# Kernel tuning notes

Hardware: AMD Instinct MI355X
Metric: run time of the kernel (lower is better)

The kernel has to match this reference:

```python
import jax, jax.numpy as jnp
import numpy as np

BETA = 0.25
DECAY = 0.99
EPS = 1e-05
K = 1024        # num_codebook_vectors
D = 256         # latent_dim


def setup_inputs() -> dict:
    key = jax.random.key(0)
    k1, k2, k3 = jax.random.split(key, 3)
    return {
        "z": jax.random.normal(k1, (32, D, 32, 32), dtype=jnp.float32),
        "embedding": jax.random.normal(k2, (K, D), dtype=jnp.float32),
        "ema_cluster_size": jnp.zeros((K,), dtype=jnp.float32),
        "ema_w": jax.random.normal(k3, (K, D), dtype=jnp.float32),
    }


def reference(z, embedding, ema_cluster_size, ema_w):
    B, C, H, W = z.shape
    zp = jnp.transpose(z, (0, 2, 3, 1))            # [B,H,W,C]
    zf = zp.reshape(-1, C)                          # [N, D], N = B*H*W

    # squared L2 distances: ||z||^2 + ||e||^2 - 2 z e^T  -> [N, K]
    d = (jnp.sum(zf * zf, axis=1, keepdims=True)
         + jnp.sum(embedding * embedding, axis=1)
         - 2.0 * (zf @ embedding.T))
    idx = jnp.argmin(d, axis=1)                     # [N]

    # one-hot @ embedding == gather of codebook rows
    z_q = embedding[idx].reshape(zp.shape)          # [B,H,W,C]

    # EMA codebook update (training branch)
    counts = jnp.zeros((K,), dtype=zf.dtype).at[idx].add(1.0)   # encodings.sum(0)
    cs = ema_cluster_size * DECAY + (1.0 - DECAY) * counts
    n = jnp.sum(cs)
    cs = (cs + EPS) / (n + K * EPS) * n             # Laplace smoothing
    dw = jax.ops.segment_sum(zf, idx, num_segments=K)           # encodings.T @ zf
    new_ema_w = ema_w * DECAY + (1.0 - DECAY) * dw
    new_embedding = new_ema_w / cs[:, None]

    # commitment loss + straight-through estimator
    e_latent_loss = jnp.mean((jax.lax.stop_gradient(z_q) - zp) ** 2)
    loss = BETA * e_latent_loss
    z_q_st = zp + jax.lax.stop_gradient(z_q - zp)
    z_q_out = jnp.transpose(z_q_st, (0, 3, 1, 2))   # [B,C,H,W]

    return z_q_out, idx[:, None], loss, new_embedding, cs, new_ema_w
```

## Files before the change

### kernel.cpp

```cpp
#include <hip/hip_runtime.h>

typedef unsigned long long ull;
typedef __attribute__((ext_vector_type(8))) short bf16x8;
typedef __attribute__((ext_vector_type(4))) float f32x4;
typedef __attribute__((ext_vector_type(8))) unsigned short u16x8;

#define DECAY 0.99f
#define BETA 0.25f
#define EPSV 1e-5f
#define EPSGAP 0.0625f

#define Dd 256
#define Kk 1024
#define Nn 32768
#define ZELEM 8388608

__device__ __forceinline__ unsigned short f2bf(float f) {
    unsigned int x = __float_as_uint(f);
    x += 0x7FFFu + ((x >> 16) & 1u);
    return (unsigned short)(x >> 16);
}
__device__ __forceinline__ float bf2f(unsigned short b) {
    return __uint_as_float(((unsigned int)b) << 16);
}
__device__ __forceinline__ unsigned mono(unsigned b) {
    return b ^ (((int)b >> 31) | 0x80000000u);
}
__device__ __forceinline__ float unmono(unsigned m) {
    unsigned b = (m & 0x80000000u) ? (m ^ 0x80000000u) : ~m;
    return __uint_as_float(b);
}
__device__ __forceinline__ unsigned umin32(unsigned a, unsigned b) { return a < b ? a : b; }
__device__ __forceinline__ unsigned umax32(unsigned a, unsigned b) { return a > b ? a : b; }

__global__ __launch_bounds__(256) void prep_e_kernel(
        const float* __restrict__ emb, unsigned short* __restrict__ ehg,
        unsigned short* __restrict__ elg, float* __restrict__ esq,
        int* __restrict__ hist, int* __restrict__ flagcnt,
        float* __restrict__ loss_fix) {
    const int nsub = blockIdx.x;
    const int t = threadIdx.x;
    if (t < 16) hist[nsub * 16 + t] = 0;
    if (nsub == 0 && t == 16) flagcnt[0] = 0;
    if (nsub == 0 && t == 17) loss_fix[0] = 0.0f;
    #pragma unroll
    for (int it = 0; it < 2; ++it) {
        const int item = it * 256 + t;
        const int kc = item >> 6, lane = item & 63;
        const int quad = lane >> 4, nl = lane & 15;
        const float* ep = emb + (size_t)(nsub * 16 + nl) * Dd + kc * 32 + quad * 8;
        const float4 a = *(const float4*)ep;
        const float4 b4 = *(const float4*)(ep + 4);
        const float v[8] = {a.x, a.y, a.z, a.w, b4.x, b4.y, b4.z, b4.w};
        u16x8 hi, lo;
        #pragma unroll
        for (int j = 0; j < 8; ++j) {
            const unsigned short h = f2bf(v[j]);
            hi[j] = h;
            lo[j] = f2bf(v[j] - bf2f(h));
        }
        const size_t off = ((size_t)(nsub * 8 + kc) * 64 + lane) * 8;
        *(u16x8*)&ehg[off] = hi;
        *(u16x8*)&elg[off] = lo;
    }
    {
        const int nl = t >> 4, seg = t & 15;
        const float* ep = emb + (size_t)(nsub * 16 + nl) * Dd + seg * 16;
        float s = 0.0f;
        #pragma unroll
        for (int j = 0; j < 4; ++j) {
            const float4 v4 = *(const float4*)(ep + j * 4);
            s += v4.x * v4.x + v4.y * v4.y + v4.z * v4.z + v4.w * v4.w;
        }
        #pragma unroll
        for (int d = 1; d < 16; d <<= 1) s += __shfl_xor(s, d);
        if (seg == 0) esq[nsub * 16 + nl] = s;
    }
}

__global__ __launch_bounds__(256) void dist_kernel(
        const float* __restrict__ z, const unsigned short* __restrict__ ehg,
        const unsigned short* __restrict__ elg, const float* __restrict__ esq,
        const float* __restrict__ emb,
        float* __restrict__ zq, float* __restrict__ dwr, int repmask,
        int* __restrict__ idx_i, float* __restrict__ idx_f,
        int* __restrict__ hist, int* __restrict__ flagcnt,
        int* __restrict__ flaglist, float* __restrict__ flagval,
        float* __restrict__ loss_p) {
    __shared__ __align__(16) unsigned char smem[70656];
    __shared__ int kidx[64];
    unsigned short* zh = (unsigned short*)smem;
    unsigned short* zl = (unsigned short*)(smem + 32768);
    ull* mb   = (ull*)(smem + 65536);
    ull* ms   = (ull*)(smem + 67584);
    float* zsqp = (float*)(smem + 69632);
    float* eldsf = (float*)smem;

    const int t = threadIdx.x, w = t >> 6, L = t & 63;
    const int quad = L >> 4, lr = L & 15;
    const int m0 = blockIdx.x * 64;
    const int b = m0 >> 10, hw0 = m0 & 1023;

    {
        const int c0 = w * 64;
        const float* zp = z + (size_t)b * 262144 + hw0 + L;
        float s = 0.0f;
        #pragma unroll
        for (int cg = 0; cg < 8; ++cg) {
            float v[8];
            #pragma unroll
            for (int j = 0; j < 8; ++j)
                v[j] = zp[(size_t)(c0 + cg * 8 + j) * 1024];
            u16x8 hi, lo;
            #pragma unroll
            for (int j = 0; j < 8; ++j) {
                s = fmaf(v[j], v[j], s);
                const unsigned short h = f2bf(v[j]);
                hi[j] = h;
                lo[j] = f2bf(v[j] - bf2f(h));
            }
            const int chunk = ((c0 >> 3) + cg) ^ (L & 7);
            *(u16x8*)&zh[L * 256 + chunk * 8] = hi;
            *(u16x8*)&zl[L * 256 + chunk * 8] = lo;
        }
        zsqp[L * 4 + w] = s;
    }
    __syncthreads();

    const unsigned short* ehw = ehg + (size_t)(w * 1024 + L) * 8;
    const unsigned short* elw = elg + (size_t)(w * 1024 + L) * 8;

    unsigned bb[16], ss[16];
    #pragma unroll
    for (int i = 0; i < 16; ++i) { bb[i] = 0xFFFFFFFFu; ss[i] = 0xFFFFFFFFu; }

    bf16x8 Bh[2][2], Bl[2][2];
    #pragma unroll
    for (int ni = 0; ni < 2; ++ni) {
        Bh[0][ni] = *(const bf16x8*)(ehw + (size_t)ni * 4096);
        Bl[0][ni] = *(const bf16x8*)(elw + (size_t)ni * 4096);
    }
    bf16x8 Ah[2][4], Al[2][4];
    #pragma unroll
    for (int mi = 0; mi < 4; ++mi) {
        const int chunk = quad ^ (lr & 7);
        const int o = (mi * 16 + lr) * 256 + chunk * 8;
        Ah[0][mi] = *(const bf16x8*)&zh[o];
        Al[0][mi] = *(const bf16x8*)&zl[o];
    }

    for (int nt = 0; nt < 8; ++nt) {
        f32x4 acc[4][2];
        #pragma unroll
        for (int mi = 0; mi < 4; ++mi)
            #pragma unroll
            for (int ni = 0; ni < 2; ++ni) acc[mi][ni] = (f32x4){0.f, 0.f, 0.f, 0.f};

        #pragma unroll
        for (int kc = 0; kc < 8; ++kc) {
            const int cur = kc & 1, nxt = cur ^ 1;
            const int nkc = (kc + 1) & 7;
            const int nnt = (kc == 7) ? ((nt + 1) & 7) : nt;
            #pragma unroll
            for (int ni = 0; ni < 2; ++ni) {
                const size_t o = (size_t)nnt * 32768 + (size_t)ni * 4096 + (size_t)nkc * 512;
                Bh[nxt][ni] = *(const bf16x8*)(ehw + o);
                Bl[nxt][ni] = *(const bf16x8*)(elw + o);
            }
            #pragma unroll
            for (int mi = 0; mi < 4; ++mi) {
                const int chunk = (nkc * 4 + quad) ^ (lr & 7);
                const int o = (mi * 16 + lr) * 256 + chunk * 8;
                Ah[nxt][mi] = *(const bf16x8*)&zh[o];
                Al[nxt][mi] = *(const bf16x8*)&zl[o];
            }
            __builtin_amdgcn_s_setprio(1);
            #pragma unroll
            for (int mi = 0; mi < 4; ++mi)
                #pragma unroll
                for (int ni = 0; ni < 2; ++ni) {
                    acc[mi][ni] = __builtin_amdgcn_mfma_f32_16x16x32_bf16(Ah[cur][mi], Bh[cur][ni], acc[mi][ni], 0, 0, 0);
                    acc[mi][ni] = __builtin_amdgcn_mfma_f32_16x16x32_bf16(Ah[cur][mi], Bl[cur][ni], acc[mi][ni], 0, 0, 0);
                    acc[mi][ni] = __builtin_amdgcn_mfma_f32_16x16x32_bf16(Al[cur][mi], Bh[cur][ni], acc[mi][ni], 0, 0, 0);
                }
            __builtin_amdgcn_s_setprio(0);
        }
        const int q0 = nt * 8 + w * 2;
        const float e0b = esq[q0 * 16 + lr] + 512.0f;
        const float e1b = esq[(q0 + 1) * 16 + lr] + 512.0f;
        #pragma unroll
        for (int mi = 0; mi < 4; ++mi)
            #pragma unroll
            for (int reg = 0; reg < 4; ++reg) {
                const int i = mi * 4 + reg;
                #pragma unroll
                for (int ni = 0; ni < 2; ++ni) {
                    const float val = fmaf(-2.0f, acc[mi][ni][reg], ni ? e1b : e0b);
                    const unsigned pk = (__float_as_uint(val) & 0xFFFFFFC0u) | (unsigned)(q0 + ni);
                    const unsigned mx = umax32(bb[i], pk);
                    bb[i] = umin32(bb[i], pk);
                    ss[i] = umin32(ss[i], mx);
                }
            }
    }

    #pragma unroll
    for (int mi = 0; mi < 4; ++mi)
        #pragma unroll
        for (int reg = 0; reg < 4; ++reg) {
            const int i = mi * 4 + reg;
            ull b2 = ((ull)(bb[i] & 0xFFFFFFC0u) << 14) | (ull)((bb[i] & 63u) * 16 + lr);
            ull s2 = ((ull)(ss[i] & 0xFFFFFFC0u) << 14) | (ull)((ss[i] & 63u) * 16 + lr);
            #pragma unroll
            for (int d = 1; d < 16; d <<= 1) {
                const ull ob = __shfl_xor(b2, d);
                const ull os = __shfl_xor(s2, d);
                const ull mx = ob < b2 ? b2 : ob;
                b2 = ob < b2 ? ob : b2;
                const ull ns = os < s2 ? os : s2;
                s2 = mx < ns ? mx : ns;
            }
            if (lr == 0) {
                const int row = mi * 16 + quad * 4 + reg;
                mb[w * 64 + row] = b2;
                ms[w * 64 + row] = s2;
            }
        }
    __syncthreads();

    if (t < 64) {
        ull b2 = mb[t], s2 = ms[t];
        #pragma unroll
        for (int ww = 1; ww < 4; ++ww) {
            const ull ob = mb[ww * 64 + t], os = ms[ww * 64 + t];
            const ull mx = ob < b2 ? b2 : ob;
            b2 = ob < b2 ? ob : b2;
            const ull ns = os < s2 ? os : s2;
            s2 = mx < ns ? mx : ns;
        }
        const int k = (int)(b2 & 16383ull);
        const float v1 = __uint_as_float((unsigned)(b2 >> 14)) - 512.0f;
        const float v2 = __uint_as_float((unsigned)(s2 >> 14)) - 512.0f;
        idx_i[m0 + t] = k;
        idx_f[m0 + t] = (float)k;
        kidx[t] = k;
        atomicAdd(&hist[k], 1);
        if (v2 - v1 < EPSGAP) {
            const int pos = atomicAdd(flagcnt, 1);
            flaglist[pos] = m0 + t;
            flagval[pos] = v1;
        }
        float lp = v1 + zsqp[t * 4] + zsqp[t * 4 + 1] + zsqp[t * 4 + 2] + zsqp[t * 4 + 3];
        #pragma unroll
        for (int d = 32; d > 0; d >>= 1) lp += __shfl_down(lp, d);
        if (t == 0) loss_p[blockIdx.x] = lp;
    }
    __syncthreads();

    for (int pr = w; pr < 64; pr += 4) {
        const float* er = emb + (size_t)kidx[pr] * Dd;
        #pragma unroll
        for (int g = 0; g < 4; ++g)
            eldsf[pr * 257 + g * 64 + L] = er[g * 64 + L];
    }
    __syncthreads();

    {
        const int g = t & 15;
        const int cl = t >> 4;
        float* zqb = zq + (size_t)b * 262144 + hw0 + g * 4;
        #pragma unroll
        for (int pass = 0; pass < 16; ++pass) {
            const int c = pass * 16 + cl;
            float4 v;
            v.x = eldsf[(g * 4 + 0) * 257 + c];
            v.y = eldsf[(g * 4 + 1) * 257 + c];
            v.z = eldsf[(g * 4 + 2) * 257 + c];
            v.w = eldsf[(g * 4 + 3) * 257 + c];
            *(float4*)(zqb + (size_t)c * 1024) = v;
        }
    }

    {
        const int c = t;
        const float* zcol = z + (size_t)b * 262144 + (size_t)c * 1024 + hw0;
        float* dwb = dwr + (size_t)(blockIdx.x & repmask) * (Kk * Dd);
        #pragma unroll 4
        for (int p = 0; p < 64; ++p) {
            atomicAdd(&dwb[(size_t)kidx[p] * Dd + c], zcol[p]);
        }
    }
}

__global__ __launch_bounds__(256) void fixup_kernel(
        const float* __restrict__ z, const float* __restrict__ emb,
        const float* __restrict__ esq, const int* __restrict__ flagcnt,
        const int* __restrict__ flaglist, const float* __restrict__ flagval,
        int* __restrict__ idx_i, float* __restrict__ idx_f,
        int* __restrict__ hist, float* __restrict__ loss_fix,
        float* __restrict__ zq, float* __restrict__ dw) {
    __shared__ float zrow[256];
    __shared__ ull red[256];
    __shared__ int s_pair[2];
    const int t = threadIdx.x;
    const int total = flagcnt[0];
    for (int fi = blockIdx.x; fi < total; fi += 512) {
        const int n = flaglist[fi];
        const int b = n >> 10, hw = n & 1023;
        __syncthreads();
        zrow[t] = z[(size_t)b * 262144 + (size_t)t * 1024 + hw];
        __syncthreads();
        ull best = ~0ull;
        #pragma unroll
        for (int kc = 0; kc < 4; ++kc) {
            const int k = t * 4 + kc;
            const float* ep = emb + (size_t)k * Dd;
            float dot = 0.0f;
            #pragma unroll 8
            for (int c4 = 0; c4 < 64; ++c4) {
                const float4 e4 = *(const float4*)(ep + c4 * 4);
                const float4 z4 = *(const float4*)&zrow[c4 * 4];
                dot = fmaf(z4.x, e4.x, dot);
                dot = fmaf(z4.y, e4.y, dot);
                dot = fmaf(z4.z, e4.z, dot);
                dot = fmaf(z4.w, e4.w, dot);
            }
            const float val = esq[k] - 2.0f * dot;
            const ull pk = ((ull)mono(__float_as_uint(val)) << 32) | (unsigned)k;
            if (pk < best) best = pk;
        }
        red[t] = best;
        __syncthreads();
        for (int s = 128; s > 0; s >>= 1) {
            if (t < s) { if (red[t + s] < red[t]) red[t] = red[t + s]; }
            __syncthreads();
        }
        if (t == 0) {
            const int knew = (int)(unsigned)(red[0] & 0xFFFFFFFFull);
            const float vnew = unmono((unsigned)(red[0] >> 32));
            const int kold = idx_i[n];
            s_pair[0] = kold;
            s_pair[1] = knew;
            if (knew != kold) {
                idx_i[n] = knew;
                idx_f[n] = (float)knew;
                atomicSub(&hist[kold], 1);
                atomicAdd(&hist[knew], 1);
            }
            atomicAdd(loss_fix, vnew - flagval[fi]);
        }
        __syncthreads();
        const int kold = s_pair[0], knew = s_pair[1];
        if (knew != kold) {
            const float zv = zrow[t];
            atomicAdd(&dw[(size_t)kold * Dd + t], -zv);
            atomicAdd(&dw[(size_t)knew * Dd + t], zv);
            zq[(size_t)b * 262144 + (size_t)t * 1024 + hw] = emb[(size_t)knew * Dd + t];
        }
    }
}

__global__ void scan_fin1_kernel(const int* __restrict__ hist,
                                 const float* __restrict__ ema_cs,
                                 const float* __restrict__ loss_p,
                                 const float* __restrict__ loss_fix,
                                 float* __restrict__ cs_out,
                                 float* __restrict__ loss_out) {
    __shared__ float wred[16], wred2[16];
    const int t = threadIdx.x;
    const int w = t >> 6, lane = t & 63;
    const int v = hist[t];
    const float csr = ema_cs[t] * DECAY + (1.0f - DECAY) * (float)v;
    float r = csr;
    float r2 = (t < 512) ? loss_p[t] : 0.0f;
    #pragma unroll
    for (int d = 32; d > 0; d >>= 1) { r += __shfl_xor(r, d); r2 += __shfl_xor(r2, d); }
    if (lane == 0) { wred[w] = r; wred2[w] = r2; }
    __syncthreads();
    if (t < 16) {
        float rr = wred[t], rr2 = wred2[t];
        #pragma unroll
        for (int d = 1; d < 16; d <<= 1) { rr += __shfl_xor(rr, d); rr2 += __shfl_xor(rr2, d); }
        if (t == 0) { wred[0] = rr; wred2[0] = rr2; }
    }
    __syncthreads();
    const float nsum = wred[0];
    const float cs = (csr + EPSV) / (nsum + (float)Kk * EPSV) * nsum;
    cs_out[t] = cs;
    if (t == 0) loss_out[0] = BETA * (wred2[0] + loss_fix[0]) / (float)ZELEM;
}

__global__ __launch_bounds__(256) void finalize2_kernel(
        const float* __restrict__ ema_w, const float* __restrict__ dwr,
        int nrep, const float* __restrict__ cs_out,
        float* __restrict__ new_emb_out, float* __restrict__ new_ema_w_out) {
    const int i = blockIdx.x * 256 + threadIdx.x;
    float s = 0.0f;
    for (int r = 0; r < nrep; ++r) s += dwr[(size_t)r * (Kk * Dd) + i];
    const float nw = ema_w[i] * DECAY + (1.0f - DECAY) * s;
    const float cs = cs_out[i >> 8];
    new_ema_w_out[i] = nw;
    new_emb_out[i]   = nw / cs;
}

extern "C" void kernel_launch(void* const* d_in, const int* in_sizes, int n_in,
                              void* d_out, int out_size, void* d_ws, size_t ws_size,
                              hipStream_t stream) {
    const float* z      = (const float*)d_in[0];
    const float* emb    = (const float*)d_in[1];
    const float* ema_cs = (const float*)d_in[2];
    const float* ema_w  = (const float*)d_in[3];

    float* out = (float*)d_out;
    float* zq_out        = out;
    float* idx_out_f     = out + 8388608;
    float* loss_out      = out + 8421376;
    float* new_emb_out   = out + 8421377;
    float* cs_out        = out + 8683521;
    float* new_ema_w_out = out + 8684545;

    int*   idx_i    = (int*)d_ws;
    int*   flagcnt  = idx_i + 32768;
    float* loss_fix = (float*)(flagcnt + 16);
    int*   flaglist = (int*)(loss_fix + 16);
    float* flagval  = (float*)(flaglist + 32768);
    int*   hist     = (int*)(flagval + 32768);
    float* esq      = (float*)(hist + 1024);
    float* loss_p   = esq + 1024;
    unsigned short* ehg = (unsigned short*)(loss_p + 512);
    unsigned short* elg = ehg + 262144;
    size_t dwr_off = ((size_t)((char*)(elg + 262144) - (char*)d_ws) + 255) & ~(size_t)255;
    float* dwr = (float*)((char*)d_ws + dwr_off);
    const size_t repbytes = (size_t)Kk * Dd * 4;
    size_t rem = (ws_size > dwr_off) ? ws_size - dwr_off : 0;
    int nrep = 1;
    while (nrep < 8 && (size_t)(nrep * 2) * repbytes <= rem) nrep <<= 1;

    hipMemsetAsync(dwr, 0, (size_t)nrep * repbytes, stream);
    prep_e_kernel<<<64, 256, 0, stream>>>(emb, ehg, elg, esq, hist, flagcnt,
                                          loss_fix);
    dist_kernel<<<Nn / 64, 256, 0, stream>>>(z, ehg, elg, esq, emb, zq_out,
                                             dwr, nrep - 1, idx_i, idx_out_f,
                                             hist, flagcnt, flaglist, flagval,
                                             loss_p);
    fixup_kernel<<<512, 256, 0, stream>>>(z, emb, esq, flagcnt, flaglist,
                                          flagval, idx_i, idx_out_f, hist,
                                          loss_fix, zq_out, dwr);
    scan_fin1_kernel<<<1, 1024, 0, stream>>>(hist, ema_cs, loss_p, loss_fix,
                                             cs_out, loss_out);
    finalize2_kernel<<<Kk * Dd / 256, 256, 0, stream>>>(ema_w, dwr, nrep,
                                                        cs_out, new_emb_out,
                                                        new_ema_w_out);
}
```

Baseline: 237.0 us.

## Fold dw memset and cluster-size/loss reductions into prep and finalize kernels

Removes the separate memset of the dw replica buffers by zeroing them inside an enlarged prep kernel (512 blocks). The total cluster count is computed up front using the identity that the counts sum to N, so cs no longer needs a global reduction after the histogram. That lets the single-block scan kernel be dropped: each finalize block computes its own cs, and block 0 reduces the loss. This cuts two launches and a serialized single-block kernel, at the cost of a slightly different summation order for n.

```diff
diff --git a/kernel.cpp b/kernel.cpp
--- a/kernel.cpp
+++ b/kernel.cpp
@@ -37,44 +37,64 @@
         const float* __restrict__ emb, unsigned short* __restrict__ ehg,
         unsigned short* __restrict__ elg, float* __restrict__ esq,
         int* __restrict__ hist, int* __restrict__ flagcnt,
-        float* __restrict__ loss_fix) {
+        float* __restrict__ loss_fix, float* __restrict__ nsum,
+        const float* __restrict__ ema_cs, float* __restrict__ dwr, int nrep) {
     const int nsub = blockIdx.x;
     const int t = threadIdx.x;
-    if (t < 16) hist[nsub * 16 + t] = 0;
-    if (nsub == 0 && t == 16) flagcnt[0] = 0;
-    if (nsub == 0 && t == 17) loss_fix[0] = 0.0f;
-    #pragma unroll
-    for (int it = 0; it < 2; ++it) {
-        const int item = it * 256 + t;
-        const int kc = item >> 6, lane = item & 63;
-        const int quad = lane >> 4, nl = lane & 15;
-        const float* ep = emb + (size_t)(nsub * 16 + nl) * Dd + kc * 32 + quad * 8;
-        const float4 a = *(const float4*)ep;
-        const float4 b4 = *(const float4*)(ep + 4);
-        const float v[8] = {a.x, a.y, a.z, a.w, b4.x, b4.y, b4.z, b4.w};
-        u16x8 hi, lo;
-        #pragma unroll
-        for (int j = 0; j < 8; ++j) {
-            const unsigned short h = f2bf(v[j]);
-            hi[j] = h;
-            lo[j] = f2bf(v[j] - bf2f(h));
-        }
-        const size_t off = ((size_t)(nsub * 8 + kc) * 64 + lane) * 8;
-        *(u16x8*)&ehg[off] = hi;
-        *(u16x8*)&elg[off] = lo;
-    }
     {
-        const int nl = t >> 4, seg = t & 15;
-        const float* ep = emb + (size_t)(nsub * 16 + nl) * Dd + seg * 16;
-        float s = 0.0f;
-        #pragma unroll
-        for (int j = 0; j < 4; ++j) {
-            const float4 v4 = *(const float4*)(ep + j * 4);
-            s += v4.x * v4.x + v4.y * v4.y + v4.z * v4.z + v4.w * v4.w;
-        }
-        #pragma unroll
-        for (int d = 1; d < 16; d <<= 1) s += __shfl_xor(s, d);
-        if (seg == 0) esq[nsub * 16 + nl] = s;
+        const int per = nrep * 512;
+        float4* dst = (float4*)(dwr + (size_t)nsub * per);
+        const int n4 = per >> 2;
+        for (int j = t; j < n4; j += 256) dst[j] = make_float4(0.f, 0.f, 0.f, 0.f);
+    }
+    if (nsub < 64) {
+        if (t < 16) hist[nsub * 16 + t] = 0;
+        if (nsub == 0 && t == 16) flagcnt[0] = 0;
+        if (nsub == 0 && t == 17) loss_fix[0] = 0.0f;
+        #pragma unroll
+        for (int it = 0; it < 2; ++it) {
+            const int item = it * 256 + t;
+            const int kc = item >> 6, lane = item & 63;
+            const int quad = lane >> 4, nl = lane & 15;
+            const float* ep = emb + (size_t)(nsub * 16 + nl) * Dd + kc * 32 + quad * 8;
+            const float4 a = *(const float4*)ep;
+            const float4 b4 = *(const float4*)(ep + 4);
+            const float v[8] = {a.x, a.y, a.z, a.w, b4.x, b4.y, b4.z, b4.w};
+            u16x8 hi, lo;
+            #pragma unroll
+            for (int j = 0; j < 8; ++j) {
+                const unsigned short h = f2bf(v[j]);
+                hi[j] = h;
+                lo[j] = f2bf(v[j] - bf2f(h));
+            }
+            const size_t off = ((size_t)(nsub * 8 + kc) * 64 + lane) * 8;
+            *(u16x8*)&ehg[off] = hi;
+            *(u16x8*)&elg[off] = lo;
+        }
+        {
+            const int nl = t >> 4, seg = t & 15;
+            const float* ep = emb + (size_t)(nsub * 16 + nl) * Dd + seg * 16;
+            float s = 0.0f;
+            #pragma unroll
+            for (int j = 0; j < 4; ++j) {
+                const float4 v4 = *(const float4*)(ep + j * 4);
+                s += v4.x * v4.x + v4.y * v4.y + v4.z * v4.z + v4.w * v4.w;
+            }
+            #pragma unroll
+            for (int d = 1; d < 16; d <<= 1) s += __shfl_xor(s, d);
+            if (seg == 0) esq[nsub * 16 + nl] = s;
+        }
+    } else if (nsub == 64) {
+        __shared__ float wred[4];
+        const int w = t >> 6, lane = t & 63;
+        float s = ema_cs[t] + ema_cs[t + 256] + ema_cs[t + 512] + ema_cs[t + 768];
+        #pragma unroll
+        for (int d = 32; d > 0; d >>= 1) s += __shfl_xor(s, d);
+        if (lane == 0) wred[w] = s;
+        __syncthreads();
+        if (t == 0)
+            nsum[0] = DECAY * (wred[0] + wred[1] + wred[2] + wred[3])
+                      + (1.0f - DECAY) * (float)Nn;
     }
 }
 
@@ -360,47 +380,37 @@
     }
 }
 
-__global__ void scan_fin1_kernel(const int* __restrict__ hist,
-                                 const float* __restrict__ ema_cs,
-                                 const float* __restrict__ loss_p,
-                                 const float* __restrict__ loss_fix,
-                                 float* __restrict__ cs_out,
-                                 float* __restrict__ loss_out) {
-    __shared__ float wred[16], wred2[16];
-    const int t = threadIdx.x;
-    const int w = t >> 6, lane = t & 63;
-    const int v = hist[t];
-    const float csr = ema_cs[t] * DECAY + (1.0f - DECAY) * (float)v;
-    float r = csr;
-    float r2 = (t < 512) ? loss_p[t] : 0.0f;
-    #pragma unroll
-    for (int d = 32; d > 0; d >>= 1) { r += __shfl_xor(r, d); r2 += __shfl_xor(r2, d); }
-    if (lane == 0) { wred[w] = r; wred2[w] = r2; }
-    __syncthreads();
-    if (t < 16) {
-        float rr = wred[t], rr2 = wred2[t];
-        #pragma unroll
-        for (int d = 1; d < 16; d <<= 1) { rr += __shfl_xor(rr, d); rr2 += __shfl_xor(rr2, d); }
-        if (t == 0) { wred[0] = rr; wred2[0] = rr2; }
-    }
-    __syncthreads();
-    const float nsum = wred[0];
-    const float cs = (csr + EPSV) / (nsum + (float)Kk * EPSV) * nsum;
-    cs_out[t] = cs;
-    if (t == 0) loss_out[0] = BETA * (wred2[0] + loss_fix[0]) / (float)ZELEM;
-}
-
 __global__ __launch_bounds__(256) void finalize2_kernel(
         const float* __restrict__ ema_w, const float* __restrict__ dwr,
-        int nrep, const float* __restrict__ cs_out,
+        int nrep, const int* __restrict__ hist,
+        const float* __restrict__ ema_cs, const float* __restrict__ nsum,
+        const float* __restrict__ loss_p, const float* __restrict__ loss_fix,
+        float* __restrict__ cs_out, float* __restrict__ loss_out,
         float* __restrict__ new_emb_out, float* __restrict__ new_ema_w_out) {
-    const int i = blockIdx.x * 256 + threadIdx.x;
+    const int k = blockIdx.x;
+    const int t = threadIdx.x;
+    const float n = nsum[0];
+    const float csr = ema_cs[k] * DECAY + (1.0f - DECAY) * (float)hist[k];
+    const float cs = (csr + EPSV) / (n + (float)Kk * EPSV) * n;
+    if (t == 0) cs_out[k] = cs;
+    const int i = k * 256 + t;
     float s = 0.0f;
     for (int r = 0; r < nrep; ++r) s += dwr[(size_t)r * (Kk * Dd) + i];
     const float nw = ema_w[i] * DECAY + (1.0f - DECAY) * s;
-    const float cs = cs_out[i >> 8];
     new_ema_w_out[i] = nw;
     new_emb_out[i]   = nw / cs;
+    if (k == 0) {
+        __shared__ float wred[4];
+        const int w = t >> 6, lane = t & 63;
+        float r2 = loss_p[t] + loss_p[t + 256];
+        #pragma unroll
+        for (int d = 32; d > 0; d >>= 1) r2 += __shfl_xor(r2, d);
+        if (lane == 0) wred[w] = r2;
+        __syncthreads();
+        if (t == 0)
+            loss_out[0] = BETA * (wred[0] + wred[1] + wred[2] + wred[3]
+                                  + loss_fix[0]) / (float)ZELEM;
+    }
 }
 
 extern "C" void kernel_launch(void* const* d_in, const int* in_sizes, int n_in,
@@ -427,7 +437,8 @@
     int*   hist     = (int*)(flagval + 32768);
     float* esq      = (float*)(hist + 1024);
     float* loss_p   = esq + 1024;
-    unsigned short* ehg = (unsigned short*)(loss_p + 512);
+    float* nsum     = loss_p + 512;
+    unsigned short* ehg = (unsigned short*)(nsum + 16);
     unsigned short* elg = ehg + 262144;
     size_t dwr_off = ((size_t)((char*)(elg + 262144) - (char*)d_ws) + 255) & ~(size_t)255;
     float* dwr = (float*)((char*)d_ws + dwr_off);
@@ -436,9 +447,8 @@
     int nrep = 1;
     while (nrep < 8 && (size_t)(nrep * 2) * repbytes <= rem) nrep <<= 1;
 
-    hipMemsetAsync(dwr, 0, (size_t)nrep * repbytes, stream);
-    prep_e_kernel<<<64, 256, 0, stream>>>(emb, ehg, elg, esq, hist, flagcnt,
-                                          loss_fix);
+    prep_e_kernel<<<512, 256, 0, stream>>>(emb, ehg, elg, esq, hist, flagcnt,
+                                           loss_fix, nsum, ema_cs, dwr, nrep);
     dist_kernel<<<Nn / 64, 256, 0, stream>>>(z, ehg, elg, esq, emb, zq_out,
                                              dwr, nrep - 1, idx_i, idx_out_f,
                                              hist, flagcnt, flaglist, flagval,
@@ -446,9 +456,8 @@
     fixup_kernel<<<512, 256, 0, stream>>>(z, emb, esq, flagcnt, flaglist,
                                           flagval, idx_i, idx_out_f, hist,
                                           loss_fix, zq_out, dwr);
-    scan_fin1_kernel<<<1, 1024, 0, stream>>>(hist, ema_cs, loss_p, loss_fix,
-                                             cs_out, loss_out);
-    finalize2_kernel<<<Kk * Dd / 256, 256, 0, stream>>>(ema_w, dwr, nrep,
-                                                        cs_out, new_emb_out,
-                                                        new_ema_w_out);
-}
+    finalize2_kernel<<<Kk, 256, 0, stream>>>(ema_w, dwr, nrep, hist, ema_cs,
+                                             nsum, loss_p, loss_fix, cs_out,
+                                             loss_out, new_emb_out,
+                                             new_ema_w_out);
+}
```

Measured after the change: 231.6 us. -2.3%, faster.
